# Optimization experiments

Measured on AMD Instinct MI355X. Metric: run time of the kernel, lower is better.

The kernel has to match this reference:

```python
import jax, jax.numpy as jnp
import numpy as np

HEADS = 8

def setup_inputs() -> dict:
    key = jax.random.key(0)
    ks = jax.random.split(key, 6)
    b, c, h, w = 32, 64, 56, 56
    m, dim = 6, 192
    inner = HEADS * c  # 512
    return {
        "x": jax.random.normal(ks[0], (b, c, h, w), dtype=jnp.float32),
        "z": jax.random.normal(ks[1], (b, m, dim), dtype=jnp.float32),
        "Wq": jax.random.normal(ks[2], (inner, dim), dtype=jnp.float32) * 0.05,
        "bq": jax.random.normal(ks[3], (inner,), dtype=jnp.float32) * 0.05,
        "Wo": jax.random.normal(ks[4], (dim, inner), dtype=jnp.float32) * 0.05,
        "bo": jax.random.normal(ks[5], (dim,), dtype=jnp.float32) * 0.05,
    }

def reference(x, z, Wq, bq, Wo, bo):
    b, c, h, w = x.shape
    _, m, d = z.shape
    heads = HEADS
    scale = d ** (-0.5)
    # torch: x.view(b, h*w, c) on contiguous (b,c,h,w) == plain reshape (memory reinterpretation)
    xf = x.reshape(b, h * w, c)
    # torch: repeat(1,1,heads) then view(b, heads, h*w, c) -- exact reshape semantics
    kv = jnp.tile(xf, (1, 1, heads)).reshape(b, heads, h * w, c)  # K = V
    # torch Linear: z @ Wq.T + bq, then view(b, heads, m, c)
    q = (jnp.einsum('bmd,id->bmi', z, Wq) + bq).reshape(b, heads, m, c)
    dots = jnp.einsum('bhmc,bhlc->bhml', q, kv) * scale
    attn = jax.nn.softmax(dots, axis=-1)
    out = jnp.einsum('bhml,bhlc->bhmc', attn, kv)
    out = out.transpose(0, 2, 1, 3).reshape(b, m, heads * c)  # 'b h m c -> b m (h c)'
    return z + jnp.einsum('bmi,di->bmd', out, Wo) + bo
```

## Files before the change

kernel.cpp:

```cpp
#include <hip/hip_runtime.h>
#include <math.h>

#define BATCH 32
#define NHEADS 8
#define M 6
#define DIM 192
#define CDIM 64
#define INNER 512
#define LFULL 3136
#define RDIST 392
#define EPITCH 400
#define NT 1024
#define KCHUNKS 98
#define WS_FLOATS (BATCH * M * INNER)

__global__ __launch_bounds__(NT) void fused_kernel(const float* __restrict__ x,
                                                   const float* __restrict__ z,
                                                   const float* __restrict__ Wq,
                                                   const float* __restrict__ bq,
                                                   float* __restrict__ ws) {
    __shared__ float sK[RDIST * CDIM];
    __shared__ float sQ[M * CDIM];
    __shared__ float sE[M][EPITCH];
    __shared__ float sPart[16][M * CDIM];
    __shared__ float sInv[M];

    const int b   = blockIdx.x >> 3;
    const int hh  = blockIdx.x & (NHEADS - 1);
    const int tid = threadIdx.x;
    const int wave = tid >> 6;
    const int lane = tid & 63;
    const int sub  = lane & 15;
    const int grp  = lane >> 4;

    const float* K = x + (size_t)b * (LFULL * CDIM) + (size_t)hh * (RDIST * CDIM);

    {
        const char* Kb = (const char*)K;
        for (int c = wave; c < KCHUNKS; c += 16) {
            int L = (c << 10) + (lane << 4);
            int G = L ^ ((((unsigned)L >> 8) & 15) << 4);
            __builtin_amdgcn_global_load_lds(
                (const __attribute__((address_space(1))) void*)(Kb + G),
                (__attribute__((address_space(3))) void*)((char*)sK + (c << 10)),
                16, 0, 0);
        }
    }

    {
        const float4* Wq4 = (const float4*)Wq;
        const float4* zb4 = (const float4*)(z + (size_t)b * (M * DIM));
        const float inv_sqrt = rsqrtf((float)DIM);
        #pragma unroll
        for (int t = 0; t < 6; ++t) {
            int o  = ((wave * 6 + t) << 2) | grp;
            int gi = hh * (M * CDIM) + o;
            int iz = gi & (INNER - 1);
            int mz = gi >> 9;
            const float4* wr = Wq4 + (size_t)iz * (DIM / 4);
            const float4* zr = zb4 + (size_t)mz * (DIM / 4);
            float acc = 0.f;
            #pragma unroll
            for (int k2 = 0; k2 < 3; ++k2) {
                float4 wv = wr[sub + 16 * k2];
                float4 zv = zr[sub + 16 * k2];
                acc += wv.x * zv.x + wv.y * zv.y + wv.z * zv.z + wv.w * zv.w;
            }
            acc += __shfl_xor(acc, 1);
            acc += __shfl_xor(acc, 2);
            acc += __shfl_xor(acc, 4);
            acc += __shfl_xor(acc, 8);
            if (sub == 0) sQ[o] = (acc + bq[iz]) * inv_sqrt;
        }
    }
    asm volatile("s_waitcnt vmcnt(0)" ::: "memory");
    __syncthreads();

    if (tid < 2 * RDIST) {
        const int r  = tid >> 1;
        const int hf = tid & 1;
        const float4* sK4 = (const float4*)sK;
        const float4* q4  = (const float4*)sQ;
        float d[M] = {0, 0, 0, 0, 0, 0};
        #pragma unroll
        for (int j = 0; j < 8; ++j) {
            int s = hf * 8 + j;
            float4 k4 = sK4[(r << 4) + (s ^ (r & 15))];
            #pragma unroll
            for (int mm = 0; mm < M; ++mm) {
                float4 qv = q4[mm * (CDIM / 4) + s];
                d[mm] += k4.x * qv.x + k4.y * qv.y + k4.z * qv.z + k4.w * qv.w;
            }
        }
        #pragma unroll
        for (int mm = 0; mm < M; ++mm) {
            float tot = d[mm] + __shfl_xor(d[mm], 1);
            if (!hf) sE[mm][r] = __expf(tot);
        }
    }
    __syncthreads();

    if (wave < M) {
        float s = (lane < RDIST - 384) ? sE[wave][384 + lane] : 0.f;
        #pragma unroll
        for (int k = 0; k < 6; ++k) s += sE[wave][lane + 64 * k];
        #pragma unroll
        for (int off = 32; off; off >>= 1) s += __shfl_xor(s, off);
        if (lane == 0) sInv[wave] = 1.0f / s;
    }

    {
        float acc[M] = {0, 0, 0, 0, 0, 0};
        for (int r = wave; r < RDIST; r += 16) {
            float kv = sK[(r << 6) + (lane ^ ((r & 15) << 2))];
            #pragma unroll
            for (int mm = 0; mm < M; ++mm) acc[mm] += sE[mm][r] * kv;
        }
        #pragma unroll
        for (int mm = 0; mm < M; ++mm) sPart[wave][mm * CDIM + lane] = acc[mm];
    }
    __syncthreads();

    if (tid < M * CDIM) {
        float v = 0.f;
        #pragma unroll
        for (int g = 0; g < 16; ++g) v += sPart[g][tid];
        v *= sInv[tid >> 6];
        const int mm = tid >> 6;
        const int c  = tid & 63;
        ws[(size_t)(b * M + mm) * INNER + hh * CDIM + c] = v;
    }
}

__global__ __launch_bounds__(256) void oproj_kernel(const float* __restrict__ ws,
                                                    const float* __restrict__ z,
                                                    const float* __restrict__ Wo,
                                                    const float* __restrict__ bo,
                                                    float* __restrict__ out) {
    __shared__ float sW[M * INNER];
    const int bb  = blockIdx.x / 6;
    const int dg  = blockIdx.x % 6;
    const int tid = threadIdx.x;

    {
        const float4* ws4 = (const float4*)(ws + (size_t)bb * (M * INNER));
        float4* sW4w = (float4*)sW;
        #pragma unroll
        for (int t = 0; t < 3; ++t) sW4w[tid + 256 * t] = ws4[tid + 256 * t];
    }
    __syncthreads();

    const int g   = tid >> 4;
    const int sub = tid & 15;
    const float4* sW4 = (const float4*)sW;
    #pragma unroll
    for (int pass = 0; pass < 2; ++pass) {
        const int d = dg * 32 + pass * 16 + g;
        const float4* wo4 = (const float4*)Wo + (size_t)d * (INNER / 4);
        float4 wv[8];
        #pragma unroll
        for (int kk = 0; kk < 8; ++kk) wv[kk] = wo4[sub + 16 * kk];
        #pragma unroll
        for (int mm = 0; mm < M; ++mm) {
            float acc = 0.f;
            #pragma unroll
            for (int kk = 0; kk < 8; ++kk) {
                float4 s4 = sW4[mm * (INNER / 4) + sub + 16 * kk];
                acc += wv[kk].x * s4.x + wv[kk].y * s4.y + wv[kk].z * s4.z + wv[kk].w * s4.w;
            }
            acc += __shfl_xor(acc, 1);
            acc += __shfl_xor(acc, 2);
            acc += __shfl_xor(acc, 4);
            acc += __shfl_xor(acc, 8);
            if (sub == mm) {
                const int oi = mm * DIM + d;
                out[(size_t)bb * (M * DIM) + oi] =
                    acc + z[(size_t)bb * (M * DIM) + oi] + bo[d];
            }
        }
    }
}

extern "C" void kernel_launch(void* const* d_in, const int* in_sizes, int n_in,
                              void* d_out, int out_size, void* d_ws, size_t ws_size,
                              hipStream_t stream) {
    const float* x  = (const float*)d_in[0];
    const float* z  = (const float*)d_in[1];
    const float* Wq = (const float*)d_in[2];
    const float* bq = (const float*)d_in[3];
    const float* Wo = (const float*)d_in[4];
    const float* bo = (const float*)d_in[5];
    float* out = (float*)d_out;
    float* ws  = (float*)d_ws;

    fused_kernel<<<BATCH * NHEADS, NT, 0, stream>>>(x, z, Wq, bq, ws);
    oproj_kernel<<<BATCH * M, 256, 0, stream>>>(ws, z, Wo, bo, out);
}
```

Baseline: 120.2 us.

## Split attention rows across two blocks and merge partial sums in output projection

Each (batch, head) attention block is split into two blocks that each take half of the 392 key rows, which doubles the grid to 512 blocks and halves the LDS footprint per block. Each half writes unnormalized partial outputs and its partial softmax denominators to the workspace. The output-projection kernel then adds the two halves and normalizes them while staging into shared memory. The aim is better CU occupancy and overlap on the 256-CU part, at the cost of extra workspace traffic and some work repeated per block (the Q projection is still computed in each half). Because the scores go through exp without subtracting a max, the two halves can be merged without any rescaling.

```diff
diff --git a/kernel.cpp b/kernel.cpp
--- a/kernel.cpp
+++ b/kernel.cpp
@@ -9,35 +9,40 @@
 #define INNER 512
 #define LFULL 3136
 #define RDIST 392
-#define EPITCH 400
+#define ROWS 196
+#define EPITCH 200
 #define NT 1024
-#define KCHUNKS 98
-#define WS_FLOATS (BATCH * M * INNER)
-
-__global__ __launch_bounds__(NT) void fused_kernel(const float* __restrict__ x,
-                                                   const float* __restrict__ z,
-                                                   const float* __restrict__ Wq,
-                                                   const float* __restrict__ bq,
-                                                   float* __restrict__ ws) {
-    __shared__ float sK[RDIST * CDIM];
+#define KCH 49
+#define PHALF 98304
+#define SOFF 196608
+#define NSUM 1536
+
+__global__ __launch_bounds__(NT) void attn_kernel(const float* __restrict__ x,
+                                                  const float* __restrict__ z,
+                                                  const float* __restrict__ Wq,
+                                                  const float* __restrict__ bq,
+                                                  float* __restrict__ ws) {
+    __shared__ float sK[ROWS * CDIM];
     __shared__ float sQ[M * CDIM];
     __shared__ float sE[M][EPITCH];
-    __shared__ float sPart[16][M * CDIM];
-    __shared__ float sInv[M];
-
-    const int b   = blockIdx.x >> 3;
-    const int hh  = blockIdx.x & (NHEADS - 1);
-    const int tid = threadIdx.x;
+    __shared__ float sPart[8][M * CDIM];
+
+    const int bid  = blockIdx.x;
+    const int half = bid & 1;
+    const int hh   = (bid >> 1) & (NHEADS - 1);
+    const int b    = bid >> 4;
+    const int tid  = threadIdx.x;
     const int wave = tid >> 6;
     const int lane = tid & 63;
     const int sub  = lane & 15;
     const int grp  = lane >> 4;
 
-    const float* K = x + (size_t)b * (LFULL * CDIM) + (size_t)hh * (RDIST * CDIM);
+    const float* K = x + (size_t)b * (LFULL * CDIM) + (size_t)hh * (RDIST * CDIM)
+                       + (size_t)half * (ROWS * CDIM);
 
     {
         const char* Kb = (const char*)K;
-        for (int c = wave; c < KCHUNKS; c += 16) {
+        for (int c = wave; c < KCH; c += 16) {
             int L = (c << 10) + (lane << 4);
             int G = L ^ ((((unsigned)L >> 8) & 15) << 4);
             __builtin_amdgcn_global_load_lds(
@@ -76,15 +81,15 @@
     asm volatile("s_waitcnt vmcnt(0)" ::: "memory");
     __syncthreads();
 
-    if (tid < 2 * RDIST) {
-        const int r  = tid >> 1;
-        const int hf = tid & 1;
+    if (tid < 4 * ROWS) {
+        const int r = tid >> 2;
+        const int q = tid & 3;
         const float4* sK4 = (const float4*)sK;
         const float4* q4  = (const float4*)sQ;
         float d[M] = {0, 0, 0, 0, 0, 0};
         #pragma unroll
-        for (int j = 0; j < 8; ++j) {
-            int s = hf * 8 + j;
+        for (int j = 0; j < 4; ++j) {
+            int s = q * 4 + j;
             float4 k4 = sK4[(r << 4) + (s ^ (r & 15))];
             #pragma unroll
             for (int mm = 0; mm < M; ++mm) {
@@ -94,24 +99,27 @@
         }
         #pragma unroll
         for (int mm = 0; mm < M; ++mm) {
-            float tot = d[mm] + __shfl_xor(d[mm], 1);
-            if (!hf) sE[mm][r] = __expf(tot);
-        }
-    }
-    __syncthreads();
-
-    if (wave < M) {
-        float s = (lane < RDIST - 384) ? sE[wave][384 + lane] : 0.f;
-        #pragma unroll
-        for (int k = 0; k < 6; ++k) s += sE[wave][lane + 64 * k];
+            float tot = d[mm];
+            tot += __shfl_xor(tot, 1);
+            tot += __shfl_xor(tot, 2);
+            if (q == 0) sE[mm][r] = __expf(tot);
+        }
+    }
+    __syncthreads();
+
+    if (wave >= 8 && wave < 8 + M) {
+        const int m = wave - 8;
+        float s = sE[m][lane] + sE[m][64 + lane] + sE[m][128 + lane]
+                + ((lane < ROWS - 192) ? sE[m][192 + lane] : 0.f);
         #pragma unroll
         for (int off = 32; off; off >>= 1) s += __shfl_xor(s, off);
-        if (lane == 0) sInv[wave] = 1.0f / s;
-    }
-
-    {
+        if (lane == 0)
+            ws[SOFF + half * NSUM + (b * NHEADS + hh) * M + m] = s;
+    }
+
+    if (wave < 8) {
         float acc[M] = {0, 0, 0, 0, 0, 0};
-        for (int r = wave; r < RDIST; r += 16) {
+        for (int r = wave; r < ROWS; r += 8) {
             float kv = sK[(r << 6) + (lane ^ ((r & 15) << 2))];
             #pragma unroll
             for (int mm = 0; mm < M; ++mm) acc[mm] += sE[mm][r] * kv;
@@ -124,11 +132,10 @@
     if (tid < M * CDIM) {
         float v = 0.f;
         #pragma unroll
-        for (int g = 0; g < 16; ++g) v += sPart[g][tid];
-        v *= sInv[tid >> 6];
+        for (int g = 0; g < 8; ++g) v += sPart[g][tid];
         const int mm = tid >> 6;
         const int c  = tid & 63;
-        ws[(size_t)(b * M + mm) * INNER + hh * CDIM + c] = v;
+        ws[half * PHALF + (size_t)(b * M + mm) * INNER + hh * CDIM + c] = v;
     }
 }
 
@@ -138,15 +145,35 @@
                                                     const float* __restrict__ bo,
                                                     float* __restrict__ out) {
     __shared__ float sW[M * INNER];
+    __shared__ float sInvB[NHEADS * M];
     const int bb  = blockIdx.x / 6;
     const int dg  = blockIdx.x % 6;
     const int tid = threadIdx.x;
 
+    if (tid < NHEADS * M) {
+        const int hh = tid / 6, m = tid % 6;
+        const float sa = ws[SOFF + (bb * NHEADS + hh) * M + m];
+        const float sb = ws[SOFF + NSUM + (bb * NHEADS + hh) * M + m];
+        sInvB[tid] = 1.0f / (sa + sb);
+    }
+    __syncthreads();
+
     {
-        const float4* ws4 = (const float4*)(ws + (size_t)bb * (M * INNER));
+        const float4* pa4 = (const float4*)(ws + (size_t)bb * (M * INNER));
+        const float4* pb4 = (const float4*)(ws + PHALF + (size_t)bb * (M * INNER));
         float4* sW4w = (float4*)sW;
         #pragma unroll
-        for (int t = 0; t < 3; ++t) sW4w[tid + 256 * t] = ws4[tid + 256 * t];
+        for (int t = 0; t < 3; ++t) {
+            const int i4 = tid + 256 * t;
+            const int m  = i4 >> 7;
+            const int hh = (i4 & 127) >> 4;
+            const float inv = sInvB[hh * 6 + m];
+            float4 a = pa4[i4], c = pb4[i4];
+            float4 v;
+            v.x = (a.x + c.x) * inv; v.y = (a.y + c.y) * inv;
+            v.z = (a.z + c.z) * inv; v.w = (a.w + c.w) * inv;
+            sW4w[i4] = v;
+        }
     }
     __syncthreads();
 
@@ -193,6 +220,6 @@
     float* out = (float*)d_out;
     float* ws  = (float*)d_ws;
 
-    fused_kernel<<<BATCH * NHEADS, NT, 0, stream>>>(x, z, Wq, bq, ws);
+    attn_kernel<<<BATCH * NHEADS * 2, NT, 0, stream>>>(x, z, Wq, bq, ws);
     oproj_kernel<<<BATCH * M, 256, 0, stream>>>(ws, z, Wo, bo, out);
 }
```

Measured after the change: 104.1 us. -13.4%, faster.
